# Performance work log

Hardware: AMD Instinct MI355X
Metric: run time of the kernel (lower is better)

## Reference

```python
import jax, jax.numpy as jnp
import numpy as np

MARGIN = 0.5
EPS = 1e-12  # matches torch F.normalize eps


def setup_inputs() -> dict:
    key = jax.random.key(0)
    embeddings = jax.random.normal(key, (8192, 256), dtype=jnp.float32)
    return {"embeddings": embeddings}


def reference(embeddings):
    n = embeddings.shape[0]
    # L2-normalize rows (torch F.normalize: x / max(||x||, eps))
    norm = jnp.linalg.norm(embeddings, axis=1, keepdims=True)
    e = embeddings / jnp.maximum(norm, EPS)
    sim = e @ e.T  # [n, n]
    # strict upper triangle mask (i < j)
    iu = jnp.triu(jnp.ones((n, n), dtype=bool), k=1)
    loss_sum = jnp.sum(jnp.where(iu, jax.nn.relu(sim - MARGIN), 0.0))
    count = n * (n - 1) // 2
    return loss_sum / count
```

## Files before the change

kernel.cpp:

```cpp
#include <hip/hip_runtime.h>
#include <hip/hip_fp16.h>

typedef __attribute__((ext_vector_type(4))) float f32x4;

#define NROWS 8192
#define DCOLS 256
#define MARGIN 0.5f
#define NT 64
#define NBLOCKS 544

__global__ __launch_bounds__(256) void norm_kernel(const float* __restrict__ x,
                                                   unsigned char* __restrict__ e) {
    const int t = threadIdx.x;
    const int l = t & 63;
    const int c = l & 31;
    const int row = blockIdx.x * 8 + (t >> 6) * 2 + (l >> 5);

    const float4 v0 = *reinterpret_cast<const float4*>(&x[row * DCOLS + c * 8]);
    const float4 v1 = *reinterpret_cast<const float4*>(&x[row * DCOLS + c * 8 + 4]);
    float ss = v0.x * v0.x + v0.y * v0.y + v0.z * v0.z + v0.w * v0.w
             + v1.x * v1.x + v1.y * v1.y + v1.z * v1.z + v1.w * v1.w;
#pragma unroll
    for (int off = 16; off >= 1; off >>= 1) ss += __shfl_xor(ss, off, 32);
    const float inv = 1.0f / fmaxf(sqrtf(ss), 1e-12f);

    const float f[8] = {v0.x, v0.y, v0.z, v0.w, v1.x, v1.y, v1.z, v1.w};
    unsigned int lo = 0, hi = 0;
#pragma unroll
    for (int i = 0; i < 4; ++i) {
        const unsigned short hb = __half_as_ushort(__float2half(f[i] * inv));
        lo |= (unsigned int)(hb >> 8) << (8 * i);
    }
#pragma unroll
    for (int i = 0; i < 4; ++i) {
        const unsigned short hb = __half_as_ushort(__float2half(f[4 + i] * inv));
        hi |= (unsigned int)(hb >> 8) << (8 * i);
    }
    uint2 o; o.x = lo; o.y = hi;
    *reinterpret_cast<uint2*>(e + (size_t)row * DCOLS + c * 8) = o;
}

__global__ __launch_bounds__(256, 3) void tile_kernel(const unsigned char* __restrict__ e,
                                                      float* __restrict__ part) {
    const int orig = blockIdx.x;
    int bb = (orig & 7) * 68 + (orig >> 3);
    int bi = 0;
    while (bb >= ((NT - bi) + 3) >> 2) { bb -= ((NT - bi) + 3) >> 2; ++bi; }
    const int j0 = bi + bb * 4;
    const int nj = min(4, NT - j0);
    const int NS = nj * 8;

    __shared__ char As[32768];
    __shared__ char Bw[4][4][1024];
    __shared__ float red[4];

    const int t = threadIdx.x;
    const int l = t & 63;
    const int w = t >> 6;
    const int wn = w;
    const int lr = l & 15;
    const int hk = l >> 4;
    const unsigned char* eA = e + (size_t)bi * 128 * DCOLS;
    const unsigned char* eB = e + (size_t)j0 * 128 * DCOLS + wn * 32 * DCOLS;
    char* myB = Bw[w][0];

#pragma unroll
    for (int i = 0; i < 8; ++i) {
        const int u = i * 256 + t;
        const int kt = u >> 8, khalf = (u >> 7) & 1, row = u & 127;
        __builtin_amdgcn_global_load_lds(
            (const __attribute__((address_space(1))) void*)(eA + row * DCOLS + kt * 32 + khalf * 16),
            (__attribute__((address_space(3))) void*)(As + u * 16), 16, 0, 0);
    }
#pragma unroll
    for (int p = 0; p < 3; ++p) {
        __builtin_amdgcn_global_load_lds(
            (const __attribute__((address_space(1))) void*)(eB + (l & 31) * DCOLS + p * 32 + (l >> 5) * 16),
            (__attribute__((address_space(3))) void*)(myB + p * 1024 + l * 16), 16, 0, 0);
    }
    asm volatile("s_waitcnt vmcnt(3)" ::: "memory");
    __builtin_amdgcn_s_barrier();
    __builtin_amdgcn_sched_barrier(0);

    f32x4 acc[8][2];
#pragma unroll
    for (int m = 0; m < 8; ++m)
#pragma unroll
        for (int n = 0; n < 2; ++n)
            acc[m][n] = (f32x4){0.f, 0.f, 0.f, 0.f};

    float local = 0.0f;
    const int rd_base = (hk >> 1) ? 1 : 0;
    for (int jx = 0; jx < nj; ++jx) {
        const int jt = j0 + jx;
#pragma unroll
        for (int kt = 0; kt < 8; ++kt) {
            const int s = jx * 8 + kt;
            asm volatile("s_waitcnt vmcnt(2)" ::: "memory");
            __builtin_amdgcn_sched_barrier(0);
            {
                int s3 = s + 3; if (s3 >= NS) s3 -= NS;
                __builtin_amdgcn_global_load_lds(
                    (const __attribute__((address_space(1))) void*)(eB
                        + (size_t)(s3 >> 3) * 128 * DCOLS
                        + (l & 31) * DCOLS + (s3 & 7) * 32 + (l >> 5) * 16),
                    (__attribute__((address_space(3))) void*)(myB + (s3 & 3) * 1024 + l * 16),
                    16, 0, 0);
            }
            long bf[2];
#pragma unroll
            for (int n = 0; n < 2; ++n)
                bf[n] = *reinterpret_cast<const long*>(
                    myB + (s & 3) * 1024 + rd_base * 512 + (n * 16 + lr) * 16 + (hk & 1) * 8);
            long af[8];
#pragma unroll
            for (int m = 0; m < 8; ++m)
                af[m] = *reinterpret_cast<const long*>(
                    As + kt * 4096 + rd_base * 2048 + (m * 16 + lr) * 16 + (hk & 1) * 8);
            __builtin_amdgcn_s_setprio(1);
#pragma unroll
            for (int m = 0; m < 8; ++m)
#pragma unroll
                for (int n = 0; n < 2; ++n)
                    acc[m][n] = __builtin_amdgcn_mfma_f32_16x16x32_bf8_bf8(
                        af[m], bf[n], acc[m][n], 0, 0, 0);
            __builtin_amdgcn_s_setprio(0);
        }
        const int gi0 = bi * 128;
        const int gj0 = jt * 128 + wn * 32;
        if (jt == bi) {
#pragma unroll
            for (int m = 0; m < 8; ++m)
#pragma unroll
                for (int n = 0; n < 2; ++n) {
#pragma unroll
                    for (int r = 0; r < 4; ++r) {
                        const int gi = gi0 + m * 16 + hk * 4 + r;
                        const int gj = gj0 + n * 16 + lr;
                        local += (gi < gj) ? fmaxf(acc[m][n][r] - MARGIN, 0.0f) : 0.0f;
                    }
                    acc[m][n] = (f32x4){0.f, 0.f, 0.f, 0.f};
                }
        } else {
#pragma unroll
            for (int m = 0; m < 8; ++m)
#pragma unroll
                for (int n = 0; n < 2; ++n) {
#pragma unroll
                    for (int r = 0; r < 4; ++r)
                        local += fmaxf(acc[m][n][r] - MARGIN, 0.0f);
                    acc[m][n] = (f32x4){0.f, 0.f, 0.f, 0.f};
                }
        }
    }

#pragma unroll
    for (int off = 32; off >= 1; off >>= 1) local += __shfl_down(local, off);
    if (l == 0) red[w] = local;
    __syncthreads();
    if (t == 0) part[orig] = red[0] + red[1] + red[2] + red[3];
}

__global__ __launch_bounds__(256) void fin_kernel(const float* __restrict__ part,
                                                  float* __restrict__ out) {
    __shared__ float red[4];
    const int t = threadIdx.x;
    float v = part[t] + part[t + 256] + (t < NBLOCKS - 512 ? part[t + 512] : 0.0f);
#pragma unroll
    for (int off = 32; off >= 1; off >>= 1) v += __shfl_down(v, off);
    if ((t & 63) == 0) red[t >> 6] = v;
    __syncthreads();
    if (t == 0) out[0] = (red[0] + red[1] + red[2] + red[3]) / 33550336.0f;
}

extern "C" void kernel_launch(void* const* d_in, const int* in_sizes, int n_in,
                              void* d_out, int out_size, void* d_ws, size_t ws_size,
                              hipStream_t stream) {
    const float* x = (const float*)d_in[0];
    float* out = (float*)d_out;
    unsigned char* e = (unsigned char*)d_ws;
    float* part = (float*)((char*)d_ws + (size_t)NROWS * DCOLS);

    norm_kernel<<<NROWS / 8, 256, 0, stream>>>(x, e);
    tile_kernel<<<NBLOCKS, 256, 0, stream>>>(e, part);
    fin_kernel<<<1, 256, 0, stream>>>(part, out);
}
```

Before: 33.19 us.

## Launch one 1024-thread block per upper-triangle tile with full A/B LDS staging

Replaces the 544-block schedule, where each 256-thread block streams up to four B tiles through a per-wave ring buffer, with 2080 blocks of 1024 threads, one per upper-triangular 128x128 tile. Each block loads A and B fully into LDS, waits once, then 16 waves each compute a 32x32 subtile. The tile index is recovered with a closed-form sqrt plus a fix-up loop. This exposes far more parallelism and removes the software pipelining, but each block reloads its A tile and has no load/compute overlap inside it. It also uses 64KB of LDS per block, which may limit how many blocks are resident.

```diff
diff --git a/kernel.cpp b/kernel.cpp
--- a/kernel.cpp
+++ b/kernel.cpp
@@ -7,7 +7,7 @@
 #define DCOLS 256
 #define MARGIN 0.5f
 #define NT 64
-#define NBLOCKS 544
+#define NBLK 2080
 
 __global__ __launch_bounds__(256) void norm_kernel(const float* __restrict__ x,
                                                    unsigned char* __restrict__ e) {
@@ -40,137 +40,133 @@
     *reinterpret_cast<uint2*>(e + (size_t)row * DCOLS + c * 8) = o;
 }
 
-__global__ __launch_bounds__(256, 3) void tile_kernel(const unsigned char* __restrict__ e,
-                                                      float* __restrict__ part) {
+__global__ __launch_bounds__(1024, 8) void tile_kernel(const unsigned char* __restrict__ e,
+                                                       float* __restrict__ part) {
     const int orig = blockIdx.x;
-    int bb = (orig & 7) * 68 + (orig >> 3);
-    int bi = 0;
-    while (bb >= ((NT - bi) + 3) >> 2) { bb -= ((NT - bi) + 3) >> 2; ++bi; }
-    const int j0 = bi + bb * 4;
-    const int nj = min(4, NT - j0);
-    const int NS = nj * 8;
+    const int t0 = (orig & 7) * 260 + (orig >> 3);
+    int bi = (int)((129.0 - sqrt(16641.0 - 8.0 * (double)t0)) * 0.5);
+    if (bi < 0) bi = 0;
+    if (bi > NT - 1) bi = NT - 1;
+#define CUM(b) (((b) * (129 - (b))) >> 1)
+    while (bi + 1 <= NT - 1 && CUM(bi + 1) <= t0) ++bi;
+    while (bi > 0 && CUM(bi) > t0) --bi;
+    const int bj = bi + (t0 - CUM(bi));
+#undef CUM
 
     __shared__ char As[32768];
-    __shared__ char Bw[4][4][1024];
-    __shared__ float red[4];
+    __shared__ char Bs[32768];
+    __shared__ float red[16];
 
     const int t = threadIdx.x;
     const int l = t & 63;
     const int w = t >> 6;
-    const int wn = w;
+    const int wm = w >> 2;
+    const int wn = w & 3;
     const int lr = l & 15;
     const int hk = l >> 4;
+
     const unsigned char* eA = e + (size_t)bi * 128 * DCOLS;
-    const unsigned char* eB = e + (size_t)j0 * 128 * DCOLS + wn * 32 * DCOLS;
-    char* myB = Bw[w][0];
+    const unsigned char* eB = e + (size_t)bj * 128 * DCOLS;
 
 #pragma unroll
-    for (int i = 0; i < 8; ++i) {
-        const int u = i * 256 + t;
-        const int kt = u >> 8, khalf = (u >> 7) & 1, row = u & 127;
+    for (int i = 0; i < 2; ++i) {
+        const int u = i * 1024 + t;
+        const int kt = u >> 8, kh = (u >> 7) & 1, row = u & 127;
         __builtin_amdgcn_global_load_lds(
-            (const __attribute__((address_space(1))) void*)(eA + row * DCOLS + kt * 32 + khalf * 16),
+            (const __attribute__((address_space(1))) void*)(eA + row * DCOLS + kt * 32 + kh * 16),
             (__attribute__((address_space(3))) void*)(As + u * 16), 16, 0, 0);
     }
 #pragma unroll
-    for (int p = 0; p < 3; ++p) {
+    for (int i = 0; i < 2; ++i) {
+        const int u = i * 1024 + t;
+        const int kt = u >> 8, kh = (u >> 7) & 1, row = u & 127;
         __builtin_amdgcn_global_load_lds(
-            (const __attribute__((address_space(1))) void*)(eB + (l & 31) * DCOLS + p * 32 + (l >> 5) * 16),
-            (__attribute__((address_space(3))) void*)(myB + p * 1024 + l * 16), 16, 0, 0);
+            (const __attribute__((address_space(1))) void*)(eB + row * DCOLS + kt * 32 + kh * 16),
+            (__attribute__((address_space(3))) void*)(Bs + u * 16), 16, 0, 0);
     }
-    asm volatile("s_waitcnt vmcnt(3)" ::: "memory");
+    asm volatile("s_waitcnt vmcnt(0)" ::: "memory");
     __builtin_amdgcn_s_barrier();
     __builtin_amdgcn_sched_barrier(0);
 
-    f32x4 acc[8][2];
+    const int ro = (hk >> 1) * 2048 + lr * 16 + (hk & 1) * 8;
+
+    f32x4 acc[2][2];
 #pragma unroll
-    for (int m = 0; m < 8; ++m)
+    for (int m = 0; m < 2; ++m)
 #pragma unroll
         for (int n = 0; n < 2; ++n)
             acc[m][n] = (f32x4){0.f, 0.f, 0.f, 0.f};
 
-    float local = 0.0f;
-    const int rd_base = (hk >> 1) ? 1 : 0;
-    for (int jx = 0; jx < nj; ++jx) {
-        const int jt = j0 + jx;
 #pragma unroll
-        for (int kt = 0; kt < 8; ++kt) {
-            const int s = jx * 8 + kt;
-            asm volatile("s_waitcnt vmcnt(2)" ::: "memory");
-            __builtin_amdgcn_sched_barrier(0);
-            {
-                int s3 = s + 3; if (s3 >= NS) s3 -= NS;
-                __builtin_amdgcn_global_load_lds(
-                    (const __attribute__((address_space(1))) void*)(eB
-                        + (size_t)(s3 >> 3) * 128 * DCOLS
-                        + (l & 31) * DCOLS + (s3 & 7) * 32 + (l >> 5) * 16),
-                    (__attribute__((address_space(3))) void*)(myB + (s3 & 3) * 1024 + l * 16),
-                    16, 0, 0);
-            }
-            long bf[2];
+    for (int kt = 0; kt < 8; ++kt) {
+        long af[2], bf[2];
+#pragma unroll
+        for (int m = 0; m < 2; ++m)
+            af[m] = *reinterpret_cast<const long*>(
+                As + kt * 4096 + (wm * 32 + m * 16) * 16 + ro);
+#pragma unroll
+        for (int n = 0; n < 2; ++n)
+            bf[n] = *reinterpret_cast<const long*>(
+                Bs + kt * 4096 + (wn * 32 + n * 16) * 16 + ro);
+#pragma unroll
+        for (int m = 0; m < 2; ++m)
 #pragma unroll
             for (int n = 0; n < 2; ++n)
-                bf[n] = *reinterpret_cast<const long*>(
-                    myB + (s & 3) * 1024 + rd_base * 512 + (n * 16 + lr) * 16 + (hk & 1) * 8);
-            long af[8];
+                acc[m][n] = __builtin_amdgcn_mfma_f32_16x16x32_bf8_bf8(
+                    af[m], bf[n], acc[m][n], 0, 0, 0);
+    }
+
+    const int gi0 = bi * 128 + wm * 32;
+    const int gj0 = bj * 128 + wn * 32;
+    float local = 0.0f;
+    if (bi == bj) {
 #pragma unroll
-            for (int m = 0; m < 8; ++m)
-                af[m] = *reinterpret_cast<const long*>(
-                    As + kt * 4096 + rd_base * 2048 + (m * 16 + lr) * 16 + (hk & 1) * 8);
-            __builtin_amdgcn_s_setprio(1);
+        for (int m = 0; m < 2; ++m)
 #pragma unroll
-            for (int m = 0; m < 8; ++m)
+            for (int n = 0; n < 2; ++n)
 #pragma unroll
-                for (int n = 0; n < 2; ++n)
-                    acc[m][n] = __builtin_amdgcn_mfma_f32_16x16x32_bf8_bf8(
-                        af[m], bf[n], acc[m][n], 0, 0, 0);
-            __builtin_amdgcn_s_setprio(0);
-        }
-        const int gi0 = bi * 128;
-        const int gj0 = jt * 128 + wn * 32;
-        if (jt == bi) {
+                for (int r = 0; r < 4; ++r) {
+                    const int gi = gi0 + m * 16 + hk * 4 + r;
+                    const int gj = gj0 + n * 16 + lr;
+                    local += (gi < gj) ? fmaxf(acc[m][n][r] - MARGIN, 0.0f) : 0.0f;
+                }
+    } else {
 #pragma unroll
-            for (int m = 0; m < 8; ++m)
+        for (int m = 0; m < 2; ++m)
 #pragma unroll
-                for (int n = 0; n < 2; ++n) {
+            for (int n = 0; n < 2; ++n)
 #pragma unroll
-                    for (int r = 0; r < 4; ++r) {
-                        const int gi = gi0 + m * 16 + hk * 4 + r;
-                        const int gj = gj0 + n * 16 + lr;
-                        local += (gi < gj) ? fmaxf(acc[m][n][r] - MARGIN, 0.0f) : 0.0f;
-                    }
-                    acc[m][n] = (f32x4){0.f, 0.f, 0.f, 0.f};
-                }
-        } else {
-#pragma unroll
-            for (int m = 0; m < 8; ++m)
-#pragma unroll
-                for (int n = 0; n < 2; ++n) {
-#pragma unroll
-                    for (int r = 0; r < 4; ++r)
-                        local += fmaxf(acc[m][n][r] - MARGIN, 0.0f);
-                    acc[m][n] = (f32x4){0.f, 0.f, 0.f, 0.f};
-                }
-        }
+                for (int r = 0; r < 4; ++r)
+                    local += fmaxf(acc[m][n][r] - MARGIN, 0.0f);
     }
 
 #pragma unroll
     for (int off = 32; off >= 1; off >>= 1) local += __shfl_down(local, off);
     if (l == 0) red[w] = local;
     __syncthreads();
-    if (t == 0) part[orig] = red[0] + red[1] + red[2] + red[3];
+    if (t == 0) {
+        float s = 0.0f;
+#pragma unroll
+        for (int i = 0; i < 16; ++i) s += red[i];
+        part[orig] = s;
+    }
 }
 
-__global__ __launch_bounds__(256) void fin_kernel(const float* __restrict__ part,
-                                                  float* __restrict__ out) {
-    __shared__ float red[4];
+__global__ __launch_bounds__(1024) void fin_kernel(const float* __restrict__ part,
+                                                   float* __restrict__ out) {
+    __shared__ float red[16];
     const int t = threadIdx.x;
-    float v = part[t] + part[t + 256] + (t < NBLOCKS - 512 ? part[t + 512] : 0.0f);
+    float v = part[t] + part[t + 1024] + (t < NBLK - 2048 ? part[t + 2048] : 0.0f);
 #pragma unroll
     for (int off = 32; off >= 1; off >>= 1) v += __shfl_down(v, off);
     if ((t & 63) == 0) red[t >> 6] = v;
     __syncthreads();
-    if (t == 0) out[0] = (red[0] + red[1] + red[2] + red[3]) / 33550336.0f;
+    if (t == 0) {
+        float s = 0.0f;
+#pragma unroll
+        for (int i = 0; i < 16; ++i) s += red[i];
+        out[0] = s / 33550336.0f;
+    }
 }
 
 extern "C" void kernel_launch(void* const* d_in, const int* in_sizes, int n_in,
@@ -182,6 +178,6 @@
     float* part = (float*)((char*)d_ws + (size_t)NROWS * DCOLS);
 
     norm_kernel<<<NROWS / 8, 256, 0, stream>>>(x, e);
-    tile_kernel<<<NBLOCKS, 256, 0, stream>>>(e, part);
-    fin_kernel<<<1, 256, 0, stream>>>(part, out);
+    tile_kernel<<<NBLK, 1024, 0, stream>>>(e, part);
+    fin_kernel<<<1, 1024, 0, stream>>>(part, out);
 }
```

After: 42.91 us. 1.29x slower.
